# Optimization experiments

Hardware: AMD Instinct MI355X
Metric: run time of the kernel (lower is better)

## Reference

```python
import jax, jax.numpy as jnp
import numpy as np

ALPHA, BETA, GAMMA = 1.0, 0.5, 0.1
IGNORE = 255


def setup_inputs() -> dict:
    key = jax.random.key(0)
    k1, k2, k3 = jax.random.split(key, 3)
    n, c, h, w, d = 8, 21, 512, 512, 32
    logit = jax.random.normal(k1, (n, c, h, w), dtype=jnp.float32)
    target = jax.random.randint(k2, (n, 1, h, w), 0, 21, dtype=jnp.int32)
    features_in = jax.random.normal(k3, (n, h * w, d), dtype=jnp.float32)
    return {"logit": logit, "target": target, "features_in": features_in}


def reference(logit, target, features_in):
    n, c, h, w = logit.shape
    P = h * w  # total_size per image (sum of all label counts incl. ignore)
    lab = target.reshape(n, P)
    valid = lab != IGNORE
    lab_safe = jnp.where(valid, lab, 0)
    vm = valid.astype(logit.dtype)

    # --- CE loss (mean over non-ignored pixels, as torch CrossEntropyLoss) ---
    logp = jax.nn.log_softmax(logit, axis=1).transpose(0, 2, 3, 1).reshape(n, P, c)
    ce_pix = -jnp.take_along_axis(logp, lab_safe[..., None], axis=2)[..., 0]
    CE = jnp.sum(ce_pix * vm) / jnp.maximum(jnp.sum(vm), 1.0)

    # --- per-pixel logit terms (VAR / Inter), vectorized over the python loop ---
    logit_f = logit.transpose(0, 2, 3, 1).reshape(n, P, c)  # [n,P,c]
    lg = jnp.take_along_axis(logit_f, lab_safe[..., None], axis=2)[..., 0]  # logit at own label
    VAR = jnp.sum(-lg * vm) / P
    Inter = jnp.sum((jnp.sum(logit_f, axis=-1) - lg) * vm) / P

    # --- Center loss: per-image per-class variance of features_in (segment reduce) ---
    onehot = jax.nn.one_hot(lab_safe, c, dtype=logit.dtype) * vm[..., None]  # [n,P,c]
    counts = jnp.sum(onehot, axis=1)                                    # [n,c]
    sums = jnp.einsum('npc,npd->ncd', onehot, features_in)              # class sums
    sumsq = jnp.einsum('npc,np->nc', onehot, jnp.sum(features_in ** 2, axis=-1))
    # sum ||f - mean||^2 = sum||f||^2 - ||sum f||^2 / count
    mean_term = jnp.sum(sums ** 2, axis=-1) / jnp.maximum(counts, 1.0)
    Center = jnp.sum(jnp.where(counts > 0, sumsq - mean_term, 0.0)) / P

    loss = (CE + ALPHA * VAR + BETA * Inter + GAMMA * Center) / n
    return loss
```

## Files before the change

### kernel.cpp

```cpp
#include <hip/hip_runtime.h>


constexpr int   N_IMG  = 8;
constexpr int   C_CLS  = 21;
constexpr int   P_PIX  = 512 * 512;
constexpr int   PQ     = P_PIX / 4;
constexpr int   IGN    = 255;
constexpr float ALPHA  = 1.0f, BETA = 0.5f, GAMMA = 0.1f;

constexpr int PIX_BLOCKS  = 2048;
constexpr int FEAT_BLOCKS = 1024;
constexpr int FEAT_ITERS  = 64;

constexpr int OFF_PIX  = 0;
constexpr int OFF_SSQ  = OFF_PIX + PIX_BLOCKS * 4;
constexpr int OFF_CLS  = OFF_SSQ + FEAT_BLOCKS;
constexpr int OFF_CNT  = OFF_CLS + FEAT_BLOCKS * 672;
constexpr int OFF_MEAN = OFF_CNT + PIX_BLOCKS * C_CLS;

__global__ __launch_bounds__(256, 4) void pixel_kernel(
    const float* __restrict__ logit, const int* __restrict__ target,
    float* __restrict__ ws)
{
    __shared__ int   s_hist[C_CLS];
    __shared__ float s_red[4][4];

    const int tid = threadIdx.x;
    if (tid < C_CLS) s_hist[tid] = 0;
    __syncthreads();

    const int q   = blockIdx.x * 256 + tid;
    const int img = q >> 16;
    const int pq  = q & (PQ - 1);

    const int4 t = ((const int4*)target)[(size_t)img * PQ + pq];
    const float4* lp = (const float4*)logit + (size_t)img * C_CLS * PQ + pq;

    float4 x[C_CLS];
#pragma unroll
    for (int ch = 0; ch < C_CLS; ++ch) x[ch] = lp[(size_t)ch * PQ];

    float4 s  = {0.f, 0.f, 0.f, 0.f};
    float4 sc = {0.f, 0.f, 0.f, 0.f};
    float4 lg = {0.f, 0.f, 0.f, 0.f};
#pragma unroll
    for (int ch = 0; ch < C_CLS; ++ch) {
        const float4 v = x[ch];
        s.x += __expf(v.x); s.y += __expf(v.y); s.z += __expf(v.z); s.w += __expf(v.w);
        sc.x += v.x; sc.y += v.y; sc.z += v.z; sc.w += v.w;
        lg.x = (t.x == ch) ? v.x : lg.x;
        lg.y = (t.y == ch) ? v.y : lg.y;
        lg.z = (t.z == ch) ? v.z : lg.z;
        lg.w = (t.w == ch) ? v.w : lg.w;
    }

    if (t.x != IGN) atomicAdd(&s_hist[t.x], 1);
    if (t.y != IGN) atomicAdd(&s_hist[t.y], 1);
    if (t.z != IGN) atomicAdd(&s_hist[t.z], 1);
    if (t.w != IGN) atomicAdd(&s_hist[t.w], 1);

    float ce = 0.f, vm = 0.f, var = 0.f, inter = 0.f;
    {
        const float v = (t.x != IGN) ? 1.f : 0.f;
        vm += v; ce += v * (__logf(s.x) - lg.x); var -= v * lg.x; inter += v * (sc.x - lg.x);
    }
    {
        const float v = (t.y != IGN) ? 1.f : 0.f;
        vm += v; ce += v * (__logf(s.y) - lg.y); var -= v * lg.y; inter += v * (sc.y - lg.y);
    }
    {
        const float v = (t.z != IGN) ? 1.f : 0.f;
        vm += v; ce += v * (__logf(s.z) - lg.z); var -= v * lg.z; inter += v * (sc.z - lg.z);
    }
    {
        const float v = (t.w != IGN) ? 1.f : 0.f;
        vm += v; ce += v * (__logf(s.w) - lg.w); var -= v * lg.w; inter += v * (sc.w - lg.w);
    }

    for (int off = 32; off; off >>= 1) {
        ce    += __shfl_xor(ce, off);
        vm    += __shfl_xor(vm, off);
        var   += __shfl_xor(var, off);
        inter += __shfl_xor(inter, off);
    }
    const int wv = tid >> 6;
    if ((tid & 63) == 0) {
        s_red[wv][0] = ce; s_red[wv][1] = vm; s_red[wv][2] = var; s_red[wv][3] = inter;
    }
    __syncthreads();

    if (tid < 4) {
        ws[OFF_PIX + blockIdx.x * 4 + tid] =
            s_red[0][tid] + s_red[1][tid] + s_red[2][tid] + s_red[3][tid];
    }
    if (tid < C_CLS) {
        ((int*)ws)[OFF_CNT + blockIdx.x * C_CLS + tid] = s_hist[tid];
    }
}

__global__ __launch_bounds__(256, 4) void feature_kernel(
    const float* __restrict__ feats, const int* __restrict__ target,
    float* __restrict__ ws)
{
    __shared__ float4 s_part[4][8][C_CLS];
    __shared__ float  s_red[4];

    const int tid   = threadIdx.x;
    const int img   = blockIdx.x >> 7;
    const int chunk = blockIdx.x & 127;
    const int p0    = chunk * 2048;
    const int pl    = tid >> 3;
    const int dg    = tid & 7;

    const float4* fb = (const float4*)feats + ((size_t)img * P_PIX + p0) * 8;
    const int*    tb = target + (size_t)img * P_PIX + p0;

    float4 acc[C_CLS];
#pragma unroll
    for (int c = 0; c < C_CLS; ++c) acc[c] = {0.f, 0.f, 0.f, 0.f};
    float ssq = 0.f;

    int    lab = tb[pl];
    float4 f   = fb[(size_t)pl * 8 + dg];
    for (int it = 0; it < FEAT_ITERS; ++it) {
        int    nlab = 0;
        float4 nf   = {0.f, 0.f, 0.f, 0.f};
        if (it + 1 < FEAT_ITERS) {
            nlab = tb[(it + 1) * 32 + pl];
            nf   = fb[(size_t)((it + 1) * 32 + pl) * 8 + dg];
        }
        const float vld = (lab != IGN) ? 1.f : 0.f;
        ssq += vld * (f.x * f.x + f.y * f.y + f.z * f.z + f.w * f.w);
#pragma unroll
        for (int c = 0; c < C_CLS; ++c) {
            const float m = (lab == c) ? 1.f : 0.f;
            acc[c].x += m * f.x; acc[c].y += m * f.y;
            acc[c].z += m * f.z; acc[c].w += m * f.w;
        }
        lab = nlab; f = nf;
    }

#pragma unroll
    for (int c = 0; c < C_CLS; ++c) {
        for (int off = 8; off <= 32; off <<= 1) {
            acc[c].x += __shfl_xor(acc[c].x, off);
            acc[c].y += __shfl_xor(acc[c].y, off);
            acc[c].z += __shfl_xor(acc[c].z, off);
            acc[c].w += __shfl_xor(acc[c].w, off);
        }
    }
    const int wv = tid >> 6;
    if ((tid & 63) < 8) {
#pragma unroll
        for (int c = 0; c < C_CLS; ++c) s_part[wv][dg][c] = acc[c];
    }

    for (int off = 1; off < 64; off <<= 1) ssq += __shfl_xor(ssq, off);
    if ((tid & 63) == 0) s_red[wv] = ssq;
    __syncthreads();

    if (tid < C_CLS * 8) {
        const int c = tid >> 3, g = tid & 7;
        const float4 a = s_part[0][g][c], b = s_part[1][g][c];
        const float4 d = s_part[2][g][c], e = s_part[3][g][c];
        float4 v;
        v.x = a.x + b.x + d.x + e.x;
        v.y = a.y + b.y + d.y + e.y;
        v.z = a.z + b.z + d.z + e.z;
        v.w = a.w + b.w + d.w + e.w;
        ((float4*)(ws + OFF_CLS))[(size_t)blockIdx.x * 168 + tid] = v;
    }
    if (tid == 0)
        ws[OFF_SSQ + blockIdx.x] = s_red[0] + s_red[1] + s_red[2] + s_red[3];
}

__global__ __launch_bounds__(128) void reduce_kernel(float* __restrict__ ws)
{
    __shared__ float sred[128];
    __shared__ int   s_cnt;

    const int img = blockIdx.x / C_CLS;
    const int c   = blockIdx.x % C_CLS;
    const int tid = threadIdx.x;
    const int d   = tid & 31;
    const int qq  = tid >> 5;

    if (tid == 0) s_cnt = 0;
    __syncthreads();

    int cnt = 0;
    const int* cp = (const int*)ws + OFF_CNT;
    for (int b = tid; b < 256; b += 128) cnt += cp[(img * 256 + b) * C_CLS + c];
    atomicAdd(&s_cnt, cnt);

    float s = 0.f;
    for (int b = qq; b < 128; b += 4)
        s += ws[OFF_CLS + (size_t)(img * 128 + b) * 672 + c * 32 + d];
    sred[tid] = s;
    __syncthreads();
    if (tid < 64) sred[tid] += sred[tid + 64];
    __syncthreads();
    if (tid < 32) {
        const float Sd = sred[tid] + sred[tid + 32];
        float n2 = Sd * Sd;
        for (int off = 1; off < 32; off <<= 1) n2 += __shfl_xor(n2, off);
        if (tid == 0)
            ws[OFF_MEAN + blockIdx.x] = n2 / fmaxf((float)s_cnt, 1.f);
    }
}

__global__ __launch_bounds__(256) void finalize_kernel(
    const float* __restrict__ ws, float* __restrict__ out)
{
    __shared__ float fr[4][6];
    const int tid = threadIdx.x;

    float ce = 0.f, vm = 0.f, var = 0.f, inter = 0.f, ssq = 0.f, mean = 0.f;
    for (int b = tid; b < PIX_BLOCKS; b += 256) {
        const float* p = ws + OFF_PIX + b * 4;
        ce += p[0]; vm += p[1]; var += p[2]; inter += p[3];
    }
    for (int b = tid; b < FEAT_BLOCKS; b += 256) ssq += ws[OFF_SSQ + b];
    if (tid < N_IMG * C_CLS) mean = ws[OFF_MEAN + tid];

    for (int off = 32; off; off >>= 1) {
        ce   += __shfl_xor(ce, off);   vm    += __shfl_xor(vm, off);
        var  += __shfl_xor(var, off);  inter += __shfl_xor(inter, off);
        ssq  += __shfl_xor(ssq, off);  mean  += __shfl_xor(mean, off);
    }
    const int wv = tid >> 6;
    if ((tid & 63) == 0) {
        fr[wv][0] = ce;  fr[wv][1] = vm;   fr[wv][2] = var;
        fr[wv][3] = inter; fr[wv][4] = ssq; fr[wv][5] = mean;
    }
    __syncthreads();
    if (tid == 0) {
        const float CE_s  = fr[0][0] + fr[1][0] + fr[2][0] + fr[3][0];
        const float VM    = fr[0][1] + fr[1][1] + fr[2][1] + fr[3][1];
        const float VAR_s = fr[0][2] + fr[1][2] + fr[2][2] + fr[3][2];
        const float INT_s = fr[0][3] + fr[1][3] + fr[2][3] + fr[3][3];
        const float SSQ   = fr[0][4] + fr[1][4] + fr[2][4] + fr[3][4];
        const float MEAN  = fr[0][5] + fr[1][5] + fr[2][5] + fr[3][5];
        const float invP   = 1.f / (float)P_PIX;
        const float CE     = CE_s / fmaxf(VM, 1.f);
        const float VAR    = VAR_s * invP;
        const float Inter  = INT_s * invP;
        const float Center = (SSQ - MEAN) * invP;
        out[0] = (CE + ALPHA * VAR + BETA * Inter + GAMMA * Center) / (float)N_IMG;
    }
}

extern "C" void kernel_launch(void* const* d_in, const int* in_sizes, int n_in,
                              void* d_out, int out_size, void* d_ws, size_t ws_size,
                              hipStream_t stream)
{
    const float* logit  = (const float*)d_in[0];
    const int*   target = (const int*)d_in[1];
    const float* feats  = (const float*)d_in[2];
    float* ws  = (float*)d_ws;
    float* out = (float*)d_out;

    pixel_kernel  <<<PIX_BLOCKS, 256, 0, stream>>>(logit, target, ws);
    feature_kernel<<<FEAT_BLOCKS, 256, 0, stream>>>(feats, target, ws);
    reduce_kernel <<<N_IMG * C_CLS, 128, 0, stream>>>(ws);
    finalize_kernel<<<1, 256, 0, stream>>>(ws, out);
}
```

Before: 505.1 us.

## Fuse pixel and feature kernels into one main kernel with chunked channel loads

Merges the logit/CE pixel pass and the feature class-sum pass into a single kernel of 1024 blocks, each handling the same 2048-pixel chunk of an image for both. Each block now processes two quads of pixels per thread and loads logits in groups of 7 channels instead of all 21 at once, which lowers register pressure. The reduce and finalize kernels are adjusted to the new per-block workspace layout. The goal is to drop one launch and let logit and feature streaming overlap within a block. The trade-off is fewer blocks for the pixel work and a longer, more serialized per-block body.

```diff
diff --git a/kernel.cpp b/kernel.cpp
--- a/kernel.cpp
+++ b/kernel.cpp
@@ -8,73 +8,83 @@
 constexpr int   IGN    = 255;
 constexpr float ALPHA  = 1.0f, BETA = 0.5f, GAMMA = 0.1f;
 
-constexpr int PIX_BLOCKS  = 2048;
-constexpr int FEAT_BLOCKS = 1024;
+constexpr int MAIN_BLOCKS = 1024;
 constexpr int FEAT_ITERS  = 64;
 
 constexpr int OFF_PIX  = 0;
-constexpr int OFF_SSQ  = OFF_PIX + PIX_BLOCKS * 4;
-constexpr int OFF_CLS  = OFF_SSQ + FEAT_BLOCKS;
-constexpr int OFF_CNT  = OFF_CLS + FEAT_BLOCKS * 672;
-constexpr int OFF_MEAN = OFF_CNT + PIX_BLOCKS * C_CLS;
-
-__global__ __launch_bounds__(256, 4) void pixel_kernel(
+constexpr int OFF_SSQ  = OFF_PIX + MAIN_BLOCKS * 4;
+constexpr int OFF_CLS  = OFF_SSQ + MAIN_BLOCKS;
+constexpr int OFF_CNT  = OFF_CLS + MAIN_BLOCKS * 672;
+constexpr int OFF_MEAN = OFF_CNT + MAIN_BLOCKS * C_CLS;
+
+__global__ __launch_bounds__(256, 4) void main_kernel(
     const float* __restrict__ logit, const int* __restrict__ target,
-    float* __restrict__ ws)
-{
-    __shared__ int   s_hist[C_CLS];
-    __shared__ float s_red[4][4];
-
-    const int tid = threadIdx.x;
+    const float* __restrict__ feats, float* __restrict__ ws)
+{
+    __shared__ int    s_hist[C_CLS];
+    __shared__ float  s_red[4][4];
+    __shared__ float4 s_part[4][8][C_CLS];
+    __shared__ float  s_ssq[4];
+
+    const int tid   = threadIdx.x;
+    const int img   = blockIdx.x >> 7;
+    const int chunk = blockIdx.x & 127;
+
     if (tid < C_CLS) s_hist[tid] = 0;
     __syncthreads();
 
-    const int q   = blockIdx.x * 256 + tid;
-    const int img = q >> 16;
-    const int pq  = q & (PQ - 1);
-
-    const int4 t = ((const int4*)target)[(size_t)img * PQ + pq];
-    const float4* lp = (const float4*)logit + (size_t)img * C_CLS * PQ + pq;
-
-    float4 x[C_CLS];
-#pragma unroll
-    for (int ch = 0; ch < C_CLS; ++ch) x[ch] = lp[(size_t)ch * PQ];
-
-    float4 s  = {0.f, 0.f, 0.f, 0.f};
-    float4 sc = {0.f, 0.f, 0.f, 0.f};
-    float4 lg = {0.f, 0.f, 0.f, 0.f};
-#pragma unroll
-    for (int ch = 0; ch < C_CLS; ++ch) {
-        const float4 v = x[ch];
-        s.x += __expf(v.x); s.y += __expf(v.y); s.z += __expf(v.z); s.w += __expf(v.w);
-        sc.x += v.x; sc.y += v.y; sc.z += v.z; sc.w += v.w;
-        lg.x = (t.x == ch) ? v.x : lg.x;
-        lg.y = (t.y == ch) ? v.y : lg.y;
-        lg.z = (t.z == ch) ? v.z : lg.z;
-        lg.w = (t.w == ch) ? v.w : lg.w;
-    }
-
-    if (t.x != IGN) atomicAdd(&s_hist[t.x], 1);
-    if (t.y != IGN) atomicAdd(&s_hist[t.y], 1);
-    if (t.z != IGN) atomicAdd(&s_hist[t.z], 1);
-    if (t.w != IGN) atomicAdd(&s_hist[t.w], 1);
-
     float ce = 0.f, vm = 0.f, var = 0.f, inter = 0.f;
-    {
-        const float v = (t.x != IGN) ? 1.f : 0.f;
-        vm += v; ce += v * (__logf(s.x) - lg.x); var -= v * lg.x; inter += v * (sc.x - lg.x);
-    }
-    {
-        const float v = (t.y != IGN) ? 1.f : 0.f;
-        vm += v; ce += v * (__logf(s.y) - lg.y); var -= v * lg.y; inter += v * (sc.y - lg.y);
-    }
-    {
-        const float v = (t.z != IGN) ? 1.f : 0.f;
-        vm += v; ce += v * (__logf(s.z) - lg.z); var -= v * lg.z; inter += v * (sc.z - lg.z);
-    }
-    {
-        const float v = (t.w != IGN) ? 1.f : 0.f;
-        vm += v; ce += v * (__logf(s.w) - lg.w); var -= v * lg.w; inter += v * (sc.w - lg.w);
+
+#pragma unroll 1
+    for (int qi = 0; qi < 2; ++qi) {
+        const int pq = chunk * 512 + qi * 256 + tid;
+        const int4 t = ((const int4*)target)[(size_t)img * PQ + pq];
+        const float4* lp = (const float4*)logit + (size_t)img * C_CLS * PQ + pq;
+
+        float4 s  = {0.f, 0.f, 0.f, 0.f};
+        float4 sc = {0.f, 0.f, 0.f, 0.f};
+        float4 lg = {0.f, 0.f, 0.f, 0.f};
+
+#pragma unroll 1
+        for (int cb = 0; cb < C_CLS; cb += 7) {
+            float4 x[7];
+#pragma unroll
+            for (int i = 0; i < 7; ++i) x[i] = lp[(size_t)(cb + i) * PQ];
+#pragma unroll
+            for (int i = 0; i < 7; ++i) {
+                const int ch = cb + i;
+                const float4 v = x[i];
+                s.x += __expf(v.x); s.y += __expf(v.y);
+                s.z += __expf(v.z); s.w += __expf(v.w);
+                sc.x += v.x; sc.y += v.y; sc.z += v.z; sc.w += v.w;
+                lg.x = (t.x == ch) ? v.x : lg.x;
+                lg.y = (t.y == ch) ? v.y : lg.y;
+                lg.z = (t.z == ch) ? v.z : lg.z;
+                lg.w = (t.w == ch) ? v.w : lg.w;
+            }
+        }
+
+        if (t.x != IGN) atomicAdd(&s_hist[t.x], 1);
+        if (t.y != IGN) atomicAdd(&s_hist[t.y], 1);
+        if (t.z != IGN) atomicAdd(&s_hist[t.z], 1);
+        if (t.w != IGN) atomicAdd(&s_hist[t.w], 1);
+
+        {
+            const float v = (t.x != IGN) ? 1.f : 0.f;
+            vm += v; ce += v * (__logf(s.x) - lg.x); var -= v * lg.x; inter += v * (sc.x - lg.x);
+        }
+        {
+            const float v = (t.y != IGN) ? 1.f : 0.f;
+            vm += v; ce += v * (__logf(s.y) - lg.y); var -= v * lg.y; inter += v * (sc.y - lg.y);
+        }
+        {
+            const float v = (t.z != IGN) ? 1.f : 0.f;
+            vm += v; ce += v * (__logf(s.z) - lg.z); var -= v * lg.z; inter += v * (sc.z - lg.z);
+        }
+        {
+            const float v = (t.w != IGN) ? 1.f : 0.f;
+            vm += v; ce += v * (__logf(s.w) - lg.w); var -= v * lg.w; inter += v * (sc.w - lg.w);
+        }
     }
 
     for (int off = 32; off; off >>= 1) {
@@ -96,21 +106,10 @@
     if (tid < C_CLS) {
         ((int*)ws)[OFF_CNT + blockIdx.x * C_CLS + tid] = s_hist[tid];
     }
-}
-
-__global__ __launch_bounds__(256, 4) void feature_kernel(
-    const float* __restrict__ feats, const int* __restrict__ target,
-    float* __restrict__ ws)
-{
-    __shared__ float4 s_part[4][8][C_CLS];
-    __shared__ float  s_red[4];
-
-    const int tid   = threadIdx.x;
-    const int img   = blockIdx.x >> 7;
-    const int chunk = blockIdx.x & 127;
-    const int p0    = chunk * 2048;
-    const int pl    = tid >> 3;
-    const int dg    = tid & 7;
+
+    const int p0 = chunk * 2048;
+    const int pl = tid >> 3;
+    const int dg = tid & 7;
 
     const float4* fb = (const float4*)feats + ((size_t)img * P_PIX + p0) * 8;
     const int*    tb = target + (size_t)img * P_PIX + p0;
@@ -149,14 +148,13 @@
             acc[c].w += __shfl_xor(acc[c].w, off);
         }
     }
-    const int wv = tid >> 6;
     if ((tid & 63) < 8) {
 #pragma unroll
         for (int c = 0; c < C_CLS; ++c) s_part[wv][dg][c] = acc[c];
     }
 
     for (int off = 1; off < 64; off <<= 1) ssq += __shfl_xor(ssq, off);
-    if ((tid & 63) == 0) s_red[wv] = ssq;
+    if ((tid & 63) == 0) s_ssq[wv] = ssq;
     __syncthreads();
 
     if (tid < C_CLS * 8) {
@@ -171,7 +169,7 @@
         ((float4*)(ws + OFF_CLS))[(size_t)blockIdx.x * 168 + tid] = v;
     }
     if (tid == 0)
-        ws[OFF_SSQ + blockIdx.x] = s_red[0] + s_red[1] + s_red[2] + s_red[3];
+        ws[OFF_SSQ + blockIdx.x] = s_ssq[0] + s_ssq[1] + s_ssq[2] + s_ssq[3];
 }
 
 __global__ __launch_bounds__(128) void reduce_kernel(float* __restrict__ ws)
@@ -188,10 +186,11 @@
     if (tid == 0) s_cnt = 0;
     __syncthreads();
 
-    int cnt = 0;
-    const int* cp = (const int*)ws + OFF_CNT;
-    for (int b = tid; b < 256; b += 128) cnt += cp[(img * 256 + b) * C_CLS + c];
-    atomicAdd(&s_cnt, cnt);
+    {
+        const int* cp = (const int*)ws + OFF_CNT;
+        const int cnt = cp[(img * 128 + tid) * C_CLS + c];
+        atomicAdd(&s_cnt, cnt);
+    }
 
     float s = 0.f;
     for (int b = qq; b < 128; b += 4)
@@ -216,11 +215,11 @@
     const int tid = threadIdx.x;
 
     float ce = 0.f, vm = 0.f, var = 0.f, inter = 0.f, ssq = 0.f, mean = 0.f;
-    for (int b = tid; b < PIX_BLOCKS; b += 256) {
+    for (int b = tid; b < MAIN_BLOCKS; b += 256) {
         const float* p = ws + OFF_PIX + b * 4;
         ce += p[0]; vm += p[1]; var += p[2]; inter += p[3];
-    }
-    for (int b = tid; b < FEAT_BLOCKS; b += 256) ssq += ws[OFF_SSQ + b];
+        ssq += ws[OFF_SSQ + b];
+    }
     if (tid < N_IMG * C_CLS) mean = ws[OFF_MEAN + tid];
 
     for (int off = 32; off; off >>= 1) {
@@ -260,8 +259,7 @@
     float* ws  = (float*)d_ws;
     float* out = (float*)d_out;
 
-    pixel_kernel  <<<PIX_BLOCKS, 256, 0, stream>>>(logit, target, ws);
-    feature_kernel<<<FEAT_BLOCKS, 256, 0, stream>>>(feats, target, ws);
-    reduce_kernel <<<N_IMG * C_CLS, 128, 0, stream>>>(ws);
+    main_kernel    <<<MAIN_BLOCKS, 256, 0, stream>>>(logit, target, feats, ws);
+    reduce_kernel  <<<N_IMG * C_CLS, 128, 0, stream>>>(ws);
     finalize_kernel<<<1, 256, 0, stream>>>(ws, out);
 }
```

Result: no change. 507.9 us (+0.5%).
